# Optimization experiments

Hardware: AMD Instinct MI355X
Metric: run time of the kernel (lower is better)

Reference implementation:

```python
import jax, jax.numpy as jnp
import numpy as np

HID = 128
FEAT = 16            # glob_in//(2+n_history) = (node_in-1)//4 = (edge_in-1)//4
N_GRAPHS = 512
N_NODES = 100000
N_EDGES = 400000
N_PER = 100000       # effects per branch (glob/node/edge)
A_TOTAL = 300000     # G.num_effects.sum()
EFF_PER_ACT = 4
NUM_ACTIONS = A_TOTAL // EFF_PER_ACT  # 75000 segments (static for jit)


def _lin(k, fan_in, fan_out):
    kw, kb = jax.random.split(k)
    s = 1.0 / np.sqrt(fan_in)
    W = jax.random.uniform(kw, (fan_in, fan_out), jnp.float32, -s, s)
    b = jax.random.uniform(kb, (fan_out,), jnp.float32, -s, s)
    return W, b


def setup_inputs() -> dict:
    key = jax.random.key(0)
    ks = jax.random.split(key, 16)
    globs = jax.random.normal(ks[0], (N_GRAPHS, HID), jnp.float32)
    nodes = jax.random.normal(ks[1], (N_NODES, HID), jnp.float32)
    edges = jax.random.normal(ks[2], (N_EDGES, HID), jnp.float32)
    action_globs = jax.random.normal(ks[3], (N_PER, FEAT), jnp.float32)
    action_nodes = jax.random.normal(ks[4], (N_PER, FEAT), jnp.float32)
    action_edges = jax.random.normal(ks[5], (N_PER, FEAT), jnp.float32)
    row = jax.random.randint(ks[6], (N_EDGES,), 0, N_NODES, jnp.int32)
    col = jax.random.randint(ks[7], (N_EDGES,), 0, N_NODES, jnp.int32)
    U = jax.random.randint(ks[8], (N_PER,), 0, N_GRAPHS, jnp.int32)
    V = jax.random.randint(ks[9], (N_PER,), 0, N_NODES, jnp.int32)
    E = jax.random.randint(ks[10], (N_PER,), 0, N_EDGES, jnp.int32)
    # disjoint write slots in the preallocated actions tensor
    UA = jnp.arange(N_PER, dtype=jnp.int32)
    VA = N_PER + jnp.arange(N_PER, dtype=jnp.int32)
    EA = 2 * N_PER + jnp.arange(N_PER, dtype=jnp.int32)
    # sorted per-effect action ids (4 effects per action)
    actions_batch = (jnp.arange(A_TOTAL, dtype=jnp.int32) // EFF_PER_ACT).astype(jnp.int32)
    glob_W, glob_b = _lin(ks[11], HID + FEAT, HID)
    node_W, node_b = _lin(ks[12], HID + FEAT, HID)
    e1_W, e1_b = _lin(ks[13], 2 * HID + FEAT, HID)
    e2_W, e2_b = _lin(ks[14], 2 * HID, HID)
    pol_W, pol_b = _lin(ks[15], HID, 1)
    return {
        "globs": globs, "nodes": nodes, "edges": edges,
        "action_globs": action_globs, "action_nodes": action_nodes, "action_edges": action_edges,
        "glob_W": glob_W, "glob_b": glob_b, "node_W": node_W, "node_b": node_b,
        "e1_W": e1_W, "e1_b": e1_b, "e2_W": e2_W, "e2_b": e2_b,
        "pol_W": pol_W, "pol_b": pol_b,
        "row": row, "col": col, "U": U, "UA": UA, "V": V, "VA": VA,
        "E": E, "EA": EA, "actions_batch": actions_batch,
    }


def _norm(batch):
    # torch norm(): consecutive group ids starting at batch[0]
    changed = (batch[1:] != batch[:-1]).astype(batch.dtype)
    return batch[0] + jnp.concatenate([jnp.zeros((1,), batch.dtype), jnp.cumsum(changed)])


def reference(globs, nodes, edges, action_globs, action_nodes, action_edges,
              glob_W, glob_b, node_W, node_b, e1_W, e1_b, e2_W, e2_b,
              pol_W, pol_b, row, col, U, UA, V, VA, E, EA, actions_batch):
    actions = jnp.zeros((A_TOTAL, HID), globs.dtype)
    # glob branch: gather globs -> small Linear -> index_put
    ga = jnp.concatenate([globs[U], action_globs], axis=1) @ glob_W + glob_b
    actions = actions.at[UA].set(ga)
    # node branch
    na = jnp.concatenate([nodes[V], action_nodes], axis=1) @ node_W + node_b
    actions = actions.at[VA].set(na)
    # edge branch: two chained Linears over gathered endpoint node feats
    EE = jnp.concatenate([nodes[row[E]], action_edges, nodes[col[E]]], axis=1) @ e1_W + e1_b
    ea = jnp.concatenate([edges[E], EE], axis=1) @ e2_W + e2_b
    actions = actions.at[EA].set(ea)
    # scatter_add segment reduction over action ids
    seg = _norm(actions_batch)
    agg = jax.ops.segment_sum(actions, seg, num_segments=NUM_ACTIONS)  # [NUM_ACTIONS, HID]
    return agg @ pol_W + pol_b  # [NUM_ACTIONS, 1]
```

## Files before the change

### kernel.cpp

```cpp
#include <hip/hip_runtime.h>

#define HID 128
#define FEAT 16
#define N_PER 100000
#define NUM_ACTIONS 75000
#define N_NODES 100000
#define N_GRAPHS 512

#define NSCAL_OFF 1024
#define GSCAL_OFF (NSCAL_OFF + 4 * N_NODES)

__device__ __forceinline__ float dot4(float4 a, float4 b) {
    return a.x * b.x + a.y * b.y + a.z * b.z + a.w * b.w;
}

__global__ __launch_bounds__(1024) void fold_kernel(
    const float* __restrict__ glob_W, const float* __restrict__ glob_b,
    const float* __restrict__ node_W, const float* __restrict__ node_b,
    const float* __restrict__ e1_W,  const float* __restrict__ e1_b,
    const float* __restrict__ e2_W,  const float* __restrict__ e2_b,
    const float* __restrict__ pol_W, const float* __restrict__ pol_b,
    float* __restrict__ ws)
{
    __shared__ float qEE[HID];
    const int t = threadIdx.x, wave = t >> 6, lane = t & 63;
    const float2 p2 = *(const float2*)&pol_W[2 * lane];

    for (int k = wave; k < HID; k += 16) {
        const float2 x = *(const float2*)&e2_W[(HID + k) * HID + 2 * lane];
        float acc = x.x * p2.x + x.y * p2.y;
        #pragma unroll
        for (int m = 32; m; m >>= 1) acc += __shfl_xor(acc, m);
        if (lane == 0) qEE[k] = acc;
    }
    __syncthreads();
    const float2 q2 = *(const float2*)&qEE[2 * lane];

    const int gw = blockIdx.x * 16 + wave;
    for (int d = gw; d < 692; d += 512) {
        float acc;
        if (d < 144) {
            const float2 x = *(const float2*)&glob_W[d * HID + 2 * lane];
            acc = x.x * p2.x + x.y * p2.y;
        } else if (d < 288) {
            const float2 x = *(const float2*)&node_W[(d - 144) * HID + 2 * lane];
            acc = x.x * p2.x + x.y * p2.y;
        } else if (d < 416) {
            const float2 x = *(const float2*)&e2_W[(d - 288) * HID + 2 * lane];
            acc = x.x * p2.x + x.y * p2.y;
        } else if (d < 688) {
            const float2 x = *(const float2*)&e1_W[(d - 416) * HID + 2 * lane];
            acc = x.x * q2.x + x.y * q2.y;
        } else if (d == 688) {
            const float2 x = *(const float2*)&glob_b[2 * lane];
            acc = x.x * p2.x + x.y * p2.y;
        } else if (d == 689) {
            const float2 x = *(const float2*)&node_b[2 * lane];
            acc = x.x * p2.x + x.y * p2.y;
        } else if (d == 690) {
            const float2 x1 = *(const float2*)&e1_b[2 * lane];
            const float2 x2 = *(const float2*)&e2_b[2 * lane];
            acc = x1.x * q2.x + x1.y * q2.y + x2.x * p2.x + x2.y * p2.y;
        } else {
            if (lane == 0) ws[691] = pol_b[0];
            continue;
        }
        #pragma unroll
        for (int m = 32; m; m >>= 1) acc += __shfl_xor(acc, m);
        if (lane == 0) ws[d] = acc;
    }
}

__global__ __launch_bounds__(256) void precompute_kernel(
    const float* __restrict__ nodes, const float* __restrict__ globs,
    float* __restrict__ ws)
{
    const int t = threadIdx.x, s = t & 31;
    const int h = blockIdx.x * 8 + (t >> 5);
    if (h < N_NODES) {
        const float4 fr = *(const float4*)&ws[416 + 4 * s];
        const float4 fc = *(const float4*)&ws[560 + 4 * s];
        const float4 fn = *(const float4*)&ws[144 + 4 * s];
        const float4 x  = *(const float4*)&nodes[h * HID + 4 * s];
        float ar = dot4(x, fr), ac = dot4(x, fc), an_ = dot4(x, fn);
        #pragma unroll
        for (int m = 16; m; m >>= 1) {
            ar  += __shfl_xor(ar, m);
            ac  += __shfl_xor(ac, m);
            an_ += __shfl_xor(an_, m);
        }
        if (s == 0) *(float4*)&ws[NSCAL_OFF + 4 * h] = make_float4(ar, ac, an_, 0.f);
    } else if (h < N_NODES + N_GRAPHS) {
        const int u = h - N_NODES;
        const float4 fg = *(const float4*)&ws[4 * s];
        const float4 x  = *(const float4*)&globs[u * HID + 4 * s];
        float a = dot4(x, fg);
        #pragma unroll
        for (int m = 16; m; m >>= 1) a += __shfl_xor(a, m);
        if (s == 0) ws[GSCAL_OFF + u] = a;
    }
}

__global__ __launch_bounds__(256) void actions_kernel(
    const float* __restrict__ edges,
    const float* __restrict__ ag, const float* __restrict__ an,
    const float* __restrict__ ae,
    const int* __restrict__ row, const int* __restrict__ col,
    const int* __restrict__ U, const int* __restrict__ V,
    const int* __restrict__ E,
    const float* __restrict__ ws, float* __restrict__ out)
{
    const int b    = blockIdx.x;
    const int wave = threadIdx.x >> 6;
    const int lane = threadIdx.x & 63;

    if (wave < 2) {
        const bool isg = (wave == 0);
        const int qtr = lane >> 4, ql = lane & 15;
        const int al  = 4 * b + qtr;
        const int gl  = 4 * al;
        const float* feats = isg ? ag : an;
        const int* idx     = isg ? U : V;
        const int wbase    = isg ? 0 : 144;

        const float4 f  = *(const float4*)&feats[gl * FEAT + 4 * ql];
        const float4 wf = *(const float4*)&ws[wbase + HID + 4 * (ql & 3)];
        float p = dot4(f, wf);
        if ((ql & 3) == 0) {
            const int id = idx[gl + (ql >> 2)];
            p += isg ? ws[GSCAL_OFF + id] : ws[NSCAL_OFF + 4 * id + 2];
        }
        #pragma unroll
        for (int m = 8; m; m >>= 1) p += __shfl_xor(p, m);
        if (ql == 0)
            out[(isg ? 0 : 25000) + al] = p + 4.f * ws[isg ? 688 : 689] + ws[691];
    } else {
        const int j = b + 6250 * (wave - 2);
        const int s = lane & 31;
        const int al = 2 * j + (lane >> 5);
        const int gl = 4 * al;
        const float4 we = *(const float4*)&ws[288 + 4 * s];
        int e[4];
        #pragma unroll
        for (int i = 0; i < 4; ++i) e[i] = E[gl + i];
        float p = 0.f;
        #pragma unroll
        for (int i = 0; i < 4; ++i) {
            const float4 x = *(const float4*)&edges[e[i] * HID + 4 * s];
            p += dot4(x, we);
        }
        if (s < 16) {
            const float4 f  = *(const float4*)&ae[gl * FEAT + 4 * s];
            const float4 wf = *(const float4*)&ws[544 + 4 * (s & 3)];
            p += dot4(f, wf);
        }
        if ((s & 3) == 0) {
            const int i = (s >> 2) & 3;
            if (s < 16) p += ws[NSCAL_OFF + 4 * row[e[i]] + 0];
            else        p += ws[NSCAL_OFF + 4 * col[e[i]] + 1];
        }
        #pragma unroll
        for (int m = 16; m; m >>= 1) p += __shfl_xor(p, m);
        if (s == 0) out[50000 + al] = p + 4.f * ws[690] + ws[691];
    }
}

extern "C" void kernel_launch(void* const* d_in, const int* in_sizes, int n_in,
                              void* d_out, int out_size, void* d_ws, size_t ws_size,
                              hipStream_t stream)
{
    const float* globs  = (const float*)d_in[0];
    const float* nodes  = (const float*)d_in[1];
    const float* edges  = (const float*)d_in[2];
    const float* ag     = (const float*)d_in[3];
    const float* an     = (const float*)d_in[4];
    const float* ae     = (const float*)d_in[5];
    const float* glob_W = (const float*)d_in[6];
    const float* glob_b = (const float*)d_in[7];
    const float* node_W = (const float*)d_in[8];
    const float* node_b = (const float*)d_in[9];
    const float* e1_W   = (const float*)d_in[10];
    const float* e1_b   = (const float*)d_in[11];
    const float* e2_W   = (const float*)d_in[12];
    const float* e2_b   = (const float*)d_in[13];
    const float* pol_W  = (const float*)d_in[14];
    const float* pol_b  = (const float*)d_in[15];
    const int*   row    = (const int*)d_in[16];
    const int*   col    = (const int*)d_in[17];
    const int*   U      = (const int*)d_in[18];
    const int*   V      = (const int*)d_in[20];
    const int*   E      = (const int*)d_in[22];

    float* ws  = (float*)d_ws;
    float* out = (float*)d_out;

    hipLaunchKernelGGL(fold_kernel, dim3(32), dim3(1024), 0, stream,
                       glob_W, glob_b, node_W, node_b, e1_W, e1_b, e2_W, e2_b,
                       pol_W, pol_b, ws);
    hipLaunchKernelGGL(precompute_kernel, dim3((N_NODES + N_GRAPHS + 7) / 8), dim3(256),
                       0, stream, nodes, globs, ws);
    hipLaunchKernelGGL(actions_kernel, dim3(6250), dim3(256), 0, stream,
                       edges, ag, an, ae, row, col, U, V, E, ws, out);
}
```

Before: 40.21 us.

## Move glob scalars into fold kernel, grid-stride node precompute, issue dependent gathers early

Glob scalar dot products move into the fold kernel, which computes the folded glob weight vector in shared memory so precompute no longer handles graphs. The node precompute kernel becomes a grid-stride loop with a fixed 2048-block grid and 16 lanes per node, each loading two float4s. In the actions kernel, the E indices are read as one int4 and the dependent row/col to node-scalar gathers are issued before the edge-row loads, shortening the serial latency chain. The cost is more work in the small fold kernel and changed lane mapping.

```diff
diff --git a/kernel.cpp b/kernel.cpp
--- a/kernel.cpp
+++ b/kernel.cpp
@@ -20,24 +20,27 @@
     const float* __restrict__ e1_W,  const float* __restrict__ e1_b,
     const float* __restrict__ e2_W,  const float* __restrict__ e2_b,
     const float* __restrict__ pol_W, const float* __restrict__ pol_b,
-    float* __restrict__ ws)
+    const float* __restrict__ globs, float* __restrict__ ws)
 {
     __shared__ float qEE[HID];
+    __shared__ float wgs[HID];
     const int t = threadIdx.x, wave = t >> 6, lane = t & 63;
     const float2 p2 = *(const float2*)&pol_W[2 * lane];
 
-    for (int k = wave; k < HID; k += 16) {
-        const float2 x = *(const float2*)&e2_W[(HID + k) * HID + 2 * lane];
+    for (int k = wave; k < 256; k += 16) {
+        const float* rp = (k < HID) ? &e2_W[(HID + k) * HID] : &glob_W[(k - HID) * HID];
+        const float2 x = *(const float2*)&rp[2 * lane];
         float acc = x.x * p2.x + x.y * p2.y;
         #pragma unroll
         for (int m = 32; m; m >>= 1) acc += __shfl_xor(acc, m);
-        if (lane == 0) qEE[k] = acc;
+        if (lane == 0) { if (k < HID) qEE[k] = acc; else wgs[k - HID] = acc; }
     }
     __syncthreads();
     const float2 q2 = *(const float2*)&qEE[2 * lane];
+    const float2 g2 = *(const float2*)&wgs[2 * lane];
 
     const int gw = blockIdx.x * 16 + wave;
-    for (int d = gw; d < 692; d += 512) {
+    for (int d = gw; d < 692 + N_GRAPHS; d += 512) {
         float acc;
         if (d < 144) {
             const float2 x = *(const float2*)&glob_W[d * HID + 2 * lane];
@@ -61,43 +64,48 @@
             const float2 x1 = *(const float2*)&e1_b[2 * lane];
             const float2 x2 = *(const float2*)&e2_b[2 * lane];
             acc = x1.x * q2.x + x1.y * q2.y + x2.x * p2.x + x2.y * p2.y;
-        } else {
+        } else if (d == 691) {
             if (lane == 0) ws[691] = pol_b[0];
             continue;
+        } else {
+            const float2 x = *(const float2*)&globs[(d - 692) * HID + 2 * lane];
+            acc = x.x * g2.x + x.y * g2.y;
         }
         #pragma unroll
         for (int m = 32; m; m >>= 1) acc += __shfl_xor(acc, m);
-        if (lane == 0) ws[d] = acc;
+        if (lane == 0) {
+            if (d < 692) ws[d] = acc;
+            else         ws[GSCAL_OFF + (d - 692)] = acc;
+        }
     }
 }
 
 __global__ __launch_bounds__(256) void precompute_kernel(
-    const float* __restrict__ nodes, const float* __restrict__ globs,
-    float* __restrict__ ws)
-{
-    const int t = threadIdx.x, s = t & 31;
-    const int h = blockIdx.x * 8 + (t >> 5);
-    if (h < N_NODES) {
-        const float4 fr = *(const float4*)&ws[416 + 4 * s];
-        const float4 fc = *(const float4*)&ws[560 + 4 * s];
-        const float4 fn = *(const float4*)&ws[144 + 4 * s];
-        const float4 x  = *(const float4*)&nodes[h * HID + 4 * s];
-        float ar = dot4(x, fr), ac = dot4(x, fc), an_ = dot4(x, fn);
-        #pragma unroll
-        for (int m = 16; m; m >>= 1) {
+    const float* __restrict__ nodes, float* __restrict__ ws)
+{
+    const int t = threadIdx.x, q = t & 15, quarter = t >> 4;
+    const int c1 = 4 * q, c2 = 64 + 4 * q;
+
+    const float4 wr1 = *(const float4*)&ws[416 + c1];
+    const float4 wr2 = *(const float4*)&ws[416 + c2];
+    const float4 wc1 = *(const float4*)&ws[560 + c1];
+    const float4 wc2 = *(const float4*)&ws[560 + c2];
+    const float4 wn1 = *(const float4*)&ws[144 + c1];
+    const float4 wn2 = *(const float4*)&ws[144 + c2];
+
+    for (int h = blockIdx.x * 16 + quarter; h < N_NODES; h += gridDim.x * 16) {
+        const float4 x1 = *(const float4*)&nodes[h * HID + c1];
+        const float4 x2 = *(const float4*)&nodes[h * HID + c2];
+        float ar = dot4(x1, wr1) + dot4(x2, wr2);
+        float ac = dot4(x1, wc1) + dot4(x2, wc2);
+        float an_ = dot4(x1, wn1) + dot4(x2, wn2);
+        #pragma unroll
+        for (int m = 8; m; m >>= 1) {
             ar  += __shfl_xor(ar, m);
             ac  += __shfl_xor(ac, m);
             an_ += __shfl_xor(an_, m);
         }
-        if (s == 0) *(float4*)&ws[NSCAL_OFF + 4 * h] = make_float4(ar, ac, an_, 0.f);
-    } else if (h < N_NODES + N_GRAPHS) {
-        const int u = h - N_NODES;
-        const float4 fg = *(const float4*)&ws[4 * s];
-        const float4 x  = *(const float4*)&globs[u * HID + 4 * s];
-        float a = dot4(x, fg);
-        #pragma unroll
-        for (int m = 16; m; m >>= 1) a += __shfl_xor(a, m);
-        if (s == 0) ws[GSCAL_OFF + u] = a;
+        if (q == 0) *(float4*)&ws[NSCAL_OFF + 4 * h] = make_float4(ar, ac, an_, 0.f);
     }
 }
 
@@ -123,13 +131,14 @@
         const int* idx     = isg ? U : V;
         const int wbase    = isg ? 0 : 144;
 
+        float p = 0.f;
+        if ((ql & 3) == 0) {
+            const int id = idx[gl + (ql >> 2)];
+            p = isg ? ws[GSCAL_OFF + id] : ws[NSCAL_OFF + 4 * id + 2];
+        }
         const float4 f  = *(const float4*)&feats[gl * FEAT + 4 * ql];
         const float4 wf = *(const float4*)&ws[wbase + HID + 4 * (ql & 3)];
-        float p = dot4(f, wf);
-        if ((ql & 3) == 0) {
-            const int id = idx[gl + (ql >> 2)];
-            p += isg ? ws[GSCAL_OFF + id] : ws[NSCAL_OFF + 4 * id + 2];
-        }
+        p += dot4(f, wf);
         #pragma unroll
         for (int m = 8; m; m >>= 1) p += __shfl_xor(p, m);
         if (ql == 0)
@@ -139,11 +148,17 @@
         const int s = lane & 31;
         const int al = 2 * j + (lane >> 5);
         const int gl = 4 * al;
+
+        const int4 e4 = *(const int4*)&E[gl];
+        int e[4] = { e4.x, e4.y, e4.z, e4.w };
+        float p = 0.f;
+        if (s < 8) {
+            const int ei = e[s & 3];
+            const int id = (s < 4) ? row[ei] : col[ei];
+            p = ws[NSCAL_OFF + 4 * id + ((s < 4) ? 0 : 1)];
+        }
+
         const float4 we = *(const float4*)&ws[288 + 4 * s];
-        int e[4];
-        #pragma unroll
-        for (int i = 0; i < 4; ++i) e[i] = E[gl + i];
-        float p = 0.f;
         #pragma unroll
         for (int i = 0; i < 4; ++i) {
             const float4 x = *(const float4*)&edges[e[i] * HID + 4 * s];
@@ -153,11 +168,6 @@
             const float4 f  = *(const float4*)&ae[gl * FEAT + 4 * s];
             const float4 wf = *(const float4*)&ws[544 + 4 * (s & 3)];
             p += dot4(f, wf);
-        }
-        if ((s & 3) == 0) {
-            const int i = (s >> 2) & 3;
-            if (s < 16) p += ws[NSCAL_OFF + 4 * row[e[i]] + 0];
-            else        p += ws[NSCAL_OFF + 4 * col[e[i]] + 1];
         }
         #pragma unroll
         for (int m = 16; m; m >>= 1) p += __shfl_xor(p, m);
@@ -196,9 +206,9 @@
 
     hipLaunchKernelGGL(fold_kernel, dim3(32), dim3(1024), 0, stream,
                        glob_W, glob_b, node_W, node_b, e1_W, e1_b, e2_W, e2_b,
-                       pol_W, pol_b, ws);
-    hipLaunchKernelGGL(precompute_kernel, dim3((N_NODES + N_GRAPHS + 7) / 8), dim3(256),
-                       0, stream, nodes, globs, ws);
+                       pol_W, pol_b, globs, ws);
+    hipLaunchKernelGGL(precompute_kernel, dim3(2048), dim3(256), 0, stream,
+                       nodes, ws);
     hipLaunchKernelGGL(actions_kernel, dim3(6250), dim3(256), 0, stream,
                        edges, ag, an, ae, row, col, U, V, E, ws, out);
 }
```

Measured after the change: 44.94 us. 1.12x slower.

## Use DPP reductions, restrict qEE compute to needed blocks, issue index gathers early

Applied to the files above, without the earlier changes.

Wavefront reductions now use DPP row shifts and row broadcasts instead of shfl_xor butterflies, so the sum ends up in the last lane. The fold kernel runs 44 blocks with one output per wave, and only the blocks that need the e2→pol projection compute it and hit the barrier. In the actions kernel the scalar index gathers (row/col/U/V) are issued before the feature loads, and E is read as one int4. The aim is to cut cross-lane latency and shorten dependent load chains, at the cost of relying on DPP broadcast semantics being correct.

```diff
diff --git a/kernel.cpp b/kernel.cpp
--- a/kernel.cpp
+++ b/kernel.cpp
@@ -12,6 +12,29 @@
 
 __device__ __forceinline__ float dot4(float4 a, float4 b) {
     return a.x * b.x + a.y * b.y + a.z * b.z + a.w * b.w;
+}
+
+template <int CTRL>
+__device__ __forceinline__ float dpp_mov(float x) {
+    return __int_as_float(__builtin_amdgcn_update_dpp(
+        0, __float_as_int(x), CTRL, 0xF, 0xF, true));
+}
+__device__ __forceinline__ float red16(float x) {
+    x += dpp_mov<0x111>(x);
+    x += dpp_mov<0x112>(x);
+    x += dpp_mov<0x114>(x);
+    x += dpp_mov<0x118>(x);
+    return x;
+}
+__device__ __forceinline__ float red32(float x) {
+    x = red16(x);
+    x += dpp_mov<0x142>(x);
+    return x;
+}
+__device__ __forceinline__ float red64(float x) {
+    x = red32(x);
+    x += dpp_mov<0x143>(x);
+    return x;
 }
 
 __global__ __launch_bounds__(1024) void fold_kernel(
@@ -24,20 +47,27 @@
 {
     __shared__ float qEE[HID];
     const int t = threadIdx.x, wave = t >> 6, lane = t & 63;
+    const int bid = blockIdx.x;
+
+    const bool needq = (bid >= 26 && bid <= 43);
+    if (needq) {
+        const int hw = t >> 5, s = t & 31;
+        const float4 p4 = *(const float4*)&pol_W[4 * s];
+        #pragma unroll
+        for (int r = 0; r < 4; ++r) {
+            const int k = hw + 32 * r;
+            const float4 x = *(const float4*)&e2_W[(HID + k) * HID + 4 * s];
+            float acc = red32(dot4(x, p4));
+            if (s == 31) qEE[k] = acc;
+        }
+        __syncthreads();
+    }
+
     const float2 p2 = *(const float2*)&pol_W[2 * lane];
-
-    for (int k = wave; k < HID; k += 16) {
-        const float2 x = *(const float2*)&e2_W[(HID + k) * HID + 2 * lane];
-        float acc = x.x * p2.x + x.y * p2.y;
-        #pragma unroll
-        for (int m = 32; m; m >>= 1) acc += __shfl_xor(acc, m);
-        if (lane == 0) qEE[k] = acc;
-    }
-    __syncthreads();
-    const float2 q2 = *(const float2*)&qEE[2 * lane];
-
-    const int gw = blockIdx.x * 16 + wave;
-    for (int d = gw; d < 692; d += 512) {
+    const int d = bid * 16 + wave;
+    if (d == 691) {
+        if (lane == 0) ws[691] = pol_b[0];
+    } else if (d < 692) {
         float acc;
         if (d < 144) {
             const float2 x = *(const float2*)&glob_W[d * HID + 2 * lane];
@@ -49,7 +79,8 @@
             const float2 x = *(const float2*)&e2_W[(d - 288) * HID + 2 * lane];
             acc = x.x * p2.x + x.y * p2.y;
         } else if (d < 688) {
-            const float2 x = *(const float2*)&e1_W[(d - 416) * HID + 2 * lane];
+            const float2 q2 = *(const float2*)&qEE[2 * lane];
+            const float2 x  = *(const float2*)&e1_W[(d - 416) * HID + 2 * lane];
             acc = x.x * q2.x + x.y * q2.y;
         } else if (d == 688) {
             const float2 x = *(const float2*)&glob_b[2 * lane];
@@ -57,17 +88,14 @@
         } else if (d == 689) {
             const float2 x = *(const float2*)&node_b[2 * lane];
             acc = x.x * p2.x + x.y * p2.y;
-        } else if (d == 690) {
+        } else {
+            const float2 q2 = *(const float2*)&qEE[2 * lane];
             const float2 x1 = *(const float2*)&e1_b[2 * lane];
             const float2 x2 = *(const float2*)&e2_b[2 * lane];
             acc = x1.x * q2.x + x1.y * q2.y + x2.x * p2.x + x2.y * p2.y;
-        } else {
-            if (lane == 0) ws[691] = pol_b[0];
-            continue;
-        }
-        #pragma unroll
-        for (int m = 32; m; m >>= 1) acc += __shfl_xor(acc, m);
-        if (lane == 0) ws[d] = acc;
+        }
+        acc = red64(acc);
+        if (lane == 63) ws[d] = acc;
     }
 }
 
@@ -82,22 +110,16 @@
         const float4 fc = *(const float4*)&ws[560 + 4 * s];
         const float4 fn = *(const float4*)&ws[144 + 4 * s];
         const float4 x  = *(const float4*)&nodes[h * HID + 4 * s];
-        float ar = dot4(x, fr), ac = dot4(x, fc), an_ = dot4(x, fn);
-        #pragma unroll
-        for (int m = 16; m; m >>= 1) {
-            ar  += __shfl_xor(ar, m);
-            ac  += __shfl_xor(ac, m);
-            an_ += __shfl_xor(an_, m);
-        }
-        if (s == 0) *(float4*)&ws[NSCAL_OFF + 4 * h] = make_float4(ar, ac, an_, 0.f);
+        const float ar = red32(dot4(x, fr));
+        const float ac = red32(dot4(x, fc));
+        const float az = red32(dot4(x, fn));
+        if (s == 31) *(float4*)&ws[NSCAL_OFF + 4 * h] = make_float4(ar, ac, az, 0.f);
     } else if (h < N_NODES + N_GRAPHS) {
         const int u = h - N_NODES;
         const float4 fg = *(const float4*)&ws[4 * s];
         const float4 x  = *(const float4*)&globs[u * HID + 4 * s];
-        float a = dot4(x, fg);
-        #pragma unroll
-        for (int m = 16; m; m >>= 1) a += __shfl_xor(a, m);
-        if (s == 0) ws[GSCAL_OFF + u] = a;
+        const float a = red32(dot4(x, fg));
+        if (s == 31) ws[GSCAL_OFF + u] = a;
     }
 }
 
@@ -123,27 +145,32 @@
         const int* idx     = isg ? U : V;
         const int wbase    = isg ? 0 : 144;
 
+        float p = 0.f;
+        if ((ql & 3) == 0) {
+            const int id = idx[gl + (ql >> 2)];
+            p = isg ? ws[GSCAL_OFF + id] : ws[NSCAL_OFF + 4 * id + 2];
+        }
         const float4 f  = *(const float4*)&feats[gl * FEAT + 4 * ql];
         const float4 wf = *(const float4*)&ws[wbase + HID + 4 * (ql & 3)];
-        float p = dot4(f, wf);
-        if ((ql & 3) == 0) {
-            const int id = idx[gl + (ql >> 2)];
-            p += isg ? ws[GSCAL_OFF + id] : ws[NSCAL_OFF + 4 * id + 2];
-        }
-        #pragma unroll
-        for (int m = 8; m; m >>= 1) p += __shfl_xor(p, m);
-        if (ql == 0)
+        p = red16(p + dot4(f, wf));
+        if (ql == 15)
             out[(isg ? 0 : 25000) + al] = p + 4.f * ws[isg ? 688 : 689] + ws[691];
     } else {
         const int j = b + 6250 * (wave - 2);
         const int s = lane & 31;
         const int al = 2 * j + (lane >> 5);
         const int gl = 4 * al;
+
+        const int4 e4 = *(const int4*)&E[gl];
+        const int e[4] = { e4.x, e4.y, e4.z, e4.w };
+        float p = 0.f;
+        if (s < 8) {
+            const int ei = e[s & 3];
+            const int id = (s < 4) ? row[ei] : col[ei];
+            p = ws[NSCAL_OFF + 4 * id + ((s < 4) ? 0 : 1)];
+        }
+
         const float4 we = *(const float4*)&ws[288 + 4 * s];
-        int e[4];
-        #pragma unroll
-        for (int i = 0; i < 4; ++i) e[i] = E[gl + i];
-        float p = 0.f;
         #pragma unroll
         for (int i = 0; i < 4; ++i) {
             const float4 x = *(const float4*)&edges[e[i] * HID + 4 * s];
@@ -154,14 +181,8 @@
             const float4 wf = *(const float4*)&ws[544 + 4 * (s & 3)];
             p += dot4(f, wf);
         }
-        if ((s & 3) == 0) {
-            const int i = (s >> 2) & 3;
-            if (s < 16) p += ws[NSCAL_OFF + 4 * row[e[i]] + 0];
-            else        p += ws[NSCAL_OFF + 4 * col[e[i]] + 1];
-        }
-        #pragma unroll
-        for (int m = 16; m; m >>= 1) p += __shfl_xor(p, m);
-        if (s == 0) out[50000 + al] = p + 4.f * ws[690] + ws[691];
+        p = red32(p);
+        if (s == 31) out[50000 + al] = p + 4.f * ws[690] + ws[691];
     }
 }
 
@@ -194,7 +215,7 @@
     float* ws  = (float*)d_ws;
     float* out = (float*)d_out;
 
-    hipLaunchKernelGGL(fold_kernel, dim3(32), dim3(1024), 0, stream,
+    hipLaunchKernelGGL(fold_kernel, dim3(44), dim3(1024), 0, stream,
                        glob_W, glob_b, node_W, node_b, e1_W, e1_b, e2_W, e2_b,
                        pol_W, pol_b, ws);
     hipLaunchKernelGGL(precompute_kernel, dim3((N_NODES + N_GRAPHS + 7) / 8), dim3(256),
```

Measured after the change: 37.10 us. -7.7%, faster.
